# Kernel optimization log

Measured on AMD Instinct MI355X. Metric: run time of the kernel, lower is better.

## Reference

```python
import jax, jax.numpy as jnp
import numpy as np
from jax import lax

LEAK = 0.2  # LeakyReLU negative slope used both in flow_conv and as act_type


def conv2d(x, w, b):
    # x: (N,Cin,H,W), w: (Cout,Cin,kh,kw) -> 'SAME' padding, stride 1
    out = lax.conv_general_dilated(x, w, (1, 1), 'SAME',
                                   dimension_numbers=('NCHW', 'OIHW', 'NCHW'))
    return out + b[None, :, None, None]


def leaky(x):
    return jnp.where(x >= 0, x, LEAK * x)


def bilinear_sample(im, ix, iy):
    # im: (C,H,W); ix,iy: (H,W) absolute pixel coords; zero padding (grid_sample default)
    C, H, W = im.shape
    x0 = jnp.floor(ix)
    y0 = jnp.floor(iy)

    def gather(xi, yi):
        valid = (xi >= 0) & (xi <= W - 1) & (yi >= 0) & (yi <= H - 1)
        xc = jnp.clip(xi, 0, W - 1).astype(jnp.int32)
        yc = jnp.clip(yi, 0, H - 1).astype(jnp.int32)
        return im[:, yc, xc] * valid[None].astype(im.dtype)

    wx1 = ix - x0
    wy1 = iy - y0
    wx0 = 1.0 - wx1
    wy0 = 1.0 - wy1
    return (gather(x0, y0) * (wx0 * wy0)[None]
            + gather(x0 + 1, y0) * (wx1 * wy0)[None]
            + gather(x0, y0 + 1) * (wx0 * wy1)[None]
            + gather(x0 + 1, y0 + 1) * (wx1 * wy1)[None])


def warp_all(h, flows):
    # h: (B,Ch,H,W); flows: (B,L,2,H,W). Matches warp(prev_h, -flow) with
    # torch F.grid_sample (bilinear, zero padding, align_corners=False).
    B, Ch, H, W = h.shape
    dt = h.dtype
    xx = jnp.arange(W, dtype=dt)
    yy = jnp.arange(H, dtype=dt)
    vx = xx[None, None, None, :] - flows[:, :, 0]  # grid + (-flow), x coord
    vy = yy[None, None, :, None] - flows[:, :, 1]
    xn = 2.0 * vx / max(W - 1, 1) - 1.0  # normalize to [-1,1]
    yn = 2.0 * vy / max(H - 1, 1) - 1.0
    ix = ((xn + 1.0) * W - 1.0) * 0.5  # unnormalize, align_corners=False
    iy = ((yn + 1.0) * H - 1.0) * 0.5
    samp = jax.vmap(jax.vmap(bilinear_sample, in_axes=(None, 0, 0)),
                    in_axes=(0, 0, 0))
    out = samp(h, ix, iy)  # (B,L,Ch,H,W)
    return out.reshape(B, -1, H, W)  # (B, L*Ch, H, W), same order as torch.cat


def setup_inputs() -> dict:
    key = jax.random.key(0)
    ks = jax.random.split(key, 8)
    B, S, C, H, W = 4, 6, 8, 96, 96
    Ch, L = 64, 13
    sc = lambda fan_in: 1.0 / np.sqrt(fan_in)
    return {
        'inputs': jax.random.normal(ks[0], (B, S, C, H, W), jnp.float32),
        'states': jnp.zeros((B, Ch, H, W), jnp.float32),
        'fw1': jax.random.normal(ks[1], (32, C + Ch, 3, 3), jnp.float32) * sc((C + Ch) * 9),
        'fb1': jnp.zeros((32,), jnp.float32),
        'fw2': jax.random.normal(ks[2], (2 * L, 32, 3, 3), jnp.float32) * sc(32 * 9),
        'fb2': jnp.zeros((2 * L,), jnp.float32),
        'i2h_w': jax.random.normal(ks[3], (3 * Ch, C, 3, 3), jnp.float32) * sc(C * 9),
        'i2h_b': jnp.zeros((3 * Ch,), jnp.float32),
        'ret_w': jax.random.normal(ks[4], (3 * Ch, L * Ch, 1, 1), jnp.float32) * sc(L * Ch),
        'ret_b': jnp.zeros((3 * Ch,), jnp.float32),
        'seq_len': 6,
    }


def reference(inputs, states, fw1, fb1, fw2, fb2, i2h_w, i2h_b, ret_w, ret_b, seq_len):
    B, S, C, H, W = inputs.shape
    Ch = states.shape[1]
    # precompute i2h over all timesteps (as in the torch module)
    i2h = conv2d(inputs.reshape(B * S, C, H, W), i2h_w, i2h_b)
    i2h = i2h.reshape(B, S, 3 * Ch, H, W)

    def step(h, xs):
        x_t, i2h_t = xs  # (B,C,H,W), (B,3Ch,H,W)
        f = leaky(conv2d(jnp.concatenate([x_t, h], axis=1), fw1, fb1))
        flows = conv2d(f, fw2, fb2)  # (B, 2L, H, W)
        flows = flows.reshape(B, flows.shape[1] // 2, 2, H, W)
        warped = warp_all(h, flows)  # (B, L*Ch, H, W)
        h2h = conv2d(warped, ret_w, ret_b)  # (B, 3Ch, H, W)
        i1, i2, i3 = jnp.split(i2h_t, 3, axis=1)
        h1, h2, h3 = jnp.split(h2h, 3, axis=1)
        r = jax.nn.sigmoid(i1 + h1)
        u = jax.nn.sigmoid(i2 + h2)
        m = leaky(i3 + r * h3)
        nh = u * h + (1.0 - u) * m
        return nh, nh

    xs = (jnp.moveaxis(inputs, 0, 1), jnp.moveaxis(i2h, 0, 1))  # time-major
    last_h, outs = lax.scan(step, states, xs)
    return jnp.moveaxis(outs, 0, 1), last_h  # ((B,S,Ch,H,W), (B,Ch,H,W))
```

## Files before the change

kernel.cpp:

```cpp
#include <hip/hip_runtime.h>
#include <hip/hip_bf16.h>
#include <math.h>

#define Bn 4
#define Sn 6
#define Cin 8
#define Hh 96
#define Ww 96
#define HW (Hh*Ww)
#define Chn 64
#define Ln 13
#define LCh (Ln*Chn)
#define OC3 (3*Chn)
#define LEAK 0.2f

typedef __hip_bfloat16 bf16;
typedef __attribute__((ext_vector_type(8))) short short8v;
typedef __attribute__((ext_vector_type(4))) short short4v;
typedef __attribute__((ext_vector_type(4))) float f32x4;

__device__ __forceinline__ float b2f(bf16 v){ return __bfloat162float(v); }
__device__ __forceinline__ bf16  f2b(float v){ return __float2bfloat16(v); }
__device__ __forceinline__ unsigned short bbits(bf16 v){ union{bf16 b; unsigned short s;} u; u.b=v; return u.s; }
__device__ __forceinline__ float us2f(unsigned short u){
    union{unsigned int i; float f;} x; x.i = ((unsigned)u)<<16; return x.f;
}

__device__ __forceinline__ int4 mk_meta(float fx, float fy, int xc, int y){
    float ix = ((float)xc - fx) * (96.0f/95.0f) - 0.5f;
    float iy = ((float)y  - fy) * (96.0f/95.0f) - 0.5f;
    float x0f = floorf(ix), y0f = floorf(iy);
    float wx1 = ix - x0f,  wy1 = iy - y0f;
    float wx0 = 1.f - wx1, wy0 = 1.f - wy1;
    float vx0 = (x0f >=  0.f && x0f <= 95.f) ? 1.f : 0.f;
    float vx1 = (x0f >= -1.f && x0f <= 94.f) ? 1.f : 0.f;
    float vy0 = (y0f >=  0.f && y0f <= 95.f) ? 1.f : 0.f;
    float vy1 = (y0f >= -1.f && y0f <= 94.f) ? 1.f : 0.f;
    int xi0 = (int)fminf(fmaxf(x0f,      0.f), 95.f);
    int xi1 = (int)fminf(fmaxf(x0f+1.f,  0.f), 95.f);
    int yi0 = (int)fminf(fmaxf(y0f,      0.f), 95.f);
    int yi1 = (int)fminf(fmaxf(y0f+1.f,  0.f), 95.f);
    union { _Float16 h[2]; int i; } pz, pw;
    pz.h[0] = (_Float16)(wx0*wy0*vx0*vy0);
    pz.h[1] = (_Float16)(wx1*wy0*vx1*vy0);
    pw.h[0] = (_Float16)(wx0*wy1*vx0*vy1);
    pw.h[1] = (_Float16)(wx1*wy1*vx1*vy1);
    int4 m;
    m.x = (yi0*Ww+xi0) | ((yi0*Ww+xi1)<<16);
    m.y = (yi1*Ww+xi0) | ((yi1*Ww+xi1)<<16);
    m.z = pz.i; m.w = pw.i;
    return m;
}

__global__ void k_prep(const float* __restrict__ fw1, const float* __restrict__ fw2,
                       const float* __restrict__ wi,  const float* __restrict__ rw,
                       bf16* __restrict__ W1b, bf16* __restrict__ W2b,
                       bf16* __restrict__ Wi,  bf16* __restrict__ Wb)
{
    int i = blockIdx.x*256 + threadIdx.x;
    if (i < 21504){
        int oc = i/672, k = i%672; float v = 0.f;
        if (k < 648){ int tap = k/72, ic = k%72; v = fw1[(size_t)oc*648 + ic*9 + tap]; }
        W1b[i] = f2b(v);
    } else if (i < 30720){
        int j = i-21504; int oc = j/288, k = j%288; float v = 0.f;
        if (oc < 26){ int tap = k/32, ic = k%32; v = fw2[(size_t)oc*288 + ic*9 + tap]; }
        W2b[j] = f2b(v);
    } else if (i < 49152){
        int j = i-30720; int oc = j/96, k = j%96; float v = 0.f;
        if (k < 72){ int tap = k/8, ic = k%8; v = wi[(size_t)oc*72 + ic*9 + tap]; }
        Wi[j] = f2b(v);
    } else if (i < 208896){
        int j = i-49152; Wb[j] = f2b(rw[j]);
    }
}

__global__ void k_packx(const float* __restrict__ x, bf16* __restrict__ x_hwc)
{
    __shared__ unsigned short tx[8][68];
    int bs = blockIdx.y, pix0 = blockIdx.x*64, tid = threadIdx.x;
    #pragma unroll
    for (int it=0; it<2; ++it){
        int idx = it*256 + tid, ic = idx>>6, p = idx&63;
        tx[ic][p] = bbits(f2b(x[((size_t)bs*Cin + ic)*HW + pix0 + p]));
    }
    __syncthreads();
    unsigned short* dst = (unsigned short*)x_hwc;
    #pragma unroll
    for (int it=0; it<2; ++it){
        int j = it*256 + tid, p = j>>3, c = j&7;
        dst[((size_t)bs*HW + pix0 + p)*8 + c] = tx[c][p];
    }
}

__global__ void k_packh0(const float* __restrict__ s, bf16* __restrict__ hwc)
{
    __shared__ unsigned short t[64][65];
    int b = blockIdx.y, pix0 = blockIdx.x*64, tid = threadIdx.x;
    unsigned short* dst = (unsigned short*)hwc;
    #pragma unroll
    for (int it=0; it<16; ++it){
        int idx = it*256 + tid, c = idx>>6, p = idx&63;
        t[c][p] = bbits(f2b(s[((size_t)b*Chn + c)*HW + pix0 + p]));
    }
    __syncthreads();
    #pragma unroll
    for (int it=0; it<16; ++it){
        int idx = it*256 + tid, p = idx>>6, c = idx&63;
        dst[((size_t)b*HW + pix0 + p)*Chn + c] = t[c][p];
    }
}

__global__ __launch_bounds__(384) void k_front(const bf16* __restrict__ x_hwc,
        const bf16* __restrict__ h_hwc,
        const bf16* __restrict__ Wi,  const float* __restrict__ ib,
        const bf16* __restrict__ W1b, const float* __restrict__ fb1,
        bf16* __restrict__ i2h_hwc, bf16* __restrict__ f_hwc, int t)
{
    __shared__ bf16 tile[3*98*72];
    int y = blockIdx.x, b = blockIdx.y, tid = threadIdx.x;
    const bf16* xb = x_hwc + (size_t)(b*Sn + t)*HW*8;
    const bf16* hb = h_hwc + (size_t)b*HW*64;
    for (int s = tid; s < 294; s += 384){
        int r = s/98, px = s%98 - 1, yy = y + r - 1;
        float4* dst = (float4*)&tile[s*72];
        if (yy>=0 && yy<Hh && px>=0 && px<Ww){
            size_t gp = (size_t)yy*Ww + px;
            dst[0] = *(const float4*)(xb + gp*8);
            const float4* hsrc = (const float4*)(hb + gp*64);
            #pragma unroll
            for (int q=0;q<8;++q) dst[1+q] = hsrc[q];
        } else {
            float4 z{0,0,0,0};
            #pragma unroll
            for (int q=0;q<9;++q) dst[q] = z;
        }
    }
    __syncthreads();
    int wv = tid>>6, lane = tid&63, x0 = wv*16, n = lane&15, kg = lane>>4;
    int pix = y*Ww + x0 + n;

    {
        f32x4 acc[12];
        #pragma unroll
        for (int m=0;m<12;++m) acc[m] = f32x4{0,0,0,0};
        #pragma unroll
        for (int kk=0; kk<3; ++kk){
            int g = kk*4 + kg;
            int tap = (g > 8) ? 8 : g;
            int dy = tap/3, dx = tap%3;
            short8v bv = *(const short8v*)&tile[((dy*98) + (x0+n) + dx)*72];
            #pragma unroll
            for (int m=0;m<12;++m){
                short8v av = *(const short8v*)(Wi + (size_t)(m*16 + n)*96 + g*8);
                acc[m] = __builtin_amdgcn_mfma_f32_16x16x32_bf16(av, bv, acc[m], 0,0,0);
            }
        }
        size_t prow = ((size_t)b*HW + pix)*192;
        #pragma unroll
        for (int m=0;m<12;++m){
            short4v sv;
            #pragma unroll
            for (int r=0;r<4;++r){
                int oc = m*16 + kg*4 + r;
                sv[r] = (short)bbits(f2b(acc[m][r] + ib[oc]));
            }
            *(short4v*)&i2h_hwc[prow + m*16 + kg*4] = sv;
        }
    }

    {
        f32x4 acc0{0,0,0,0}, acc1{0,0,0,0};
        #pragma unroll
        for (int kk=0; kk<21; ++kk){
            int g = kk*4 + kg;
            int gc = (g > 80) ? 80 : g;
            int tap = gc/9, ch0 = (gc%9)*8;
            int dy = tap/3, dx = tap%3;
            short8v bv = *(const short8v*)&tile[(((dy*98) + (x0+n) + dx))*72 + ch0];
            short8v a0 = *(const short8v*)(W1b + (size_t)n*672 + g*8);
            short8v a1 = *(const short8v*)(W1b + (size_t)(16+n)*672 + g*8);
            acc0 = __builtin_amdgcn_mfma_f32_16x16x32_bf16(a0, bv, acc0, 0,0,0);
            acc1 = __builtin_amdgcn_mfma_f32_16x16x32_bf16(a1, bv, acc1, 0,0,0);
        }
        size_t prow = (size_t)b*HW + pix;
        #pragma unroll
        for (int mt=0; mt<2; ++mt){
            f32x4 a = mt ? acc1 : acc0;
            short4v sv;
            #pragma unroll
            for (int r=0;r<4;++r){
                int oc = mt*16 + kg*4 + r;
                float v = a[r] + fb1[oc];
                sv[r] = (short)bbits(f2b((v >= 0.f) ? v : LEAK*v));
            }
            *(short4v*)&f_hwc[prow*32 + mt*16 + kg*4] = sv;
        }
    }
}

__global__ __launch_bounds__(384) void k_conv2meta(const bf16* __restrict__ f_hwc,
        const bf16* __restrict__ W2b, const float* __restrict__ fb2,
        int4* __restrict__ meta)
{
    __shared__ bf16 tile[3*98*32];
    int y = blockIdx.x, b = blockIdx.y, tid = threadIdx.x;
    const bf16* fb = f_hwc + (size_t)b*HW*32;
    for (int s = tid; s < 294; s += 384){
        int r = s/98, px = s%98 - 1, yy = y + r - 1;
        float4* dst = (float4*)&tile[s*32];
        if (yy>=0 && yy<Hh && px>=0 && px<Ww){
            const float4* src = (const float4*)(fb + ((size_t)yy*Ww + px)*32);
            #pragma unroll
            for (int q=0;q<4;++q) dst[q] = src[q];
        } else {
            float4 z{0,0,0,0};
            #pragma unroll
            for (int q=0;q<4;++q) dst[q] = z;
        }
    }
    __syncthreads();
    int wv = tid>>6, lane = tid&63, x0 = wv*16, n = lane&15, kg = lane>>4;
    f32x4 acc0{0,0,0,0}, acc1{0,0,0,0};
    #pragma unroll
    for (int kk=0; kk<9; ++kk){
        int g = kk*4 + kg;
        int tap = g>>2, ch0 = (g&3)*8;
        int dy = tap/3, dx = tap%3;
        short8v bv = *(const short8v*)&tile[(((dy*98) + (x0+n) + dx))*32 + ch0];
        short8v a0 = *(const short8v*)(W2b + (size_t)n*288 + g*8);
        short8v a1 = *(const short8v*)(W2b + (size_t)(16+n)*288 + g*8);
        acc0 = __builtin_amdgcn_mfma_f32_16x16x32_bf16(a0, bv, acc0, 0,0,0);
        acc1 = __builtin_amdgcn_mfma_f32_16x16x32_bf16(a1, bv, acc1, 0,0,0);
    }
    int xc = x0 + n, pix = y*Ww + xc;
    int4* mb = meta + (size_t)b*Ln*HW + pix;
    {
        float v0 = acc0[0] + fb2[kg*4+0], v1 = acc0[1] + fb2[kg*4+1];
        float v2 = acc0[2] + fb2[kg*4+2], v3 = acc0[3] + fb2[kg*4+3];
        mb[(size_t)(2*kg  )*HW] = mk_meta(v0, v1, xc, y);
        mb[(size_t)(2*kg+1)*HW] = mk_meta(v2, v3, xc, y);
    }
    if (kg < 3){
        float v0 = acc1[0] + fb2[16+kg*4+0], v1 = acc1[1] + fb2[16+kg*4+1];
        mb[(size_t)(8+2*kg)*HW] = mk_meta(v0, v1, xc, y);
        if (kg < 2){
            float v2 = acc1[2] + fb2[16+kg*4+2], v3 = acc1[3] + fb2[16+kg*4+3];
            mb[(size_t)(9+2*kg)*HW] = mk_meta(v2, v3, xc, y);
        }
    }
}

__global__ __launch_bounds__(256) void k_fused(const int4* __restrict__ meta,
        const bf16* __restrict__ h_cur, const bf16* __restrict__ Wb,
        const float* __restrict__ rb, const bf16* __restrict__ i2h_hwc,
        bf16* __restrict__ h_nxt, float* __restrict__ out, int t)
{
    __shared__ bf16 wlds[32*LCh];
    char* ldsb = (char*)wlds;
    int tid = threadIdx.x, wv = tid>>6, lane = tid&63;
    int b = blockIdx.y, pix0 = blockIdx.x*32;
    const bf16* hb = h_cur + (size_t)b*HW*64;
    const unsigned short* hsu = (const unsigned short*)hb;
    const int4* mb = meta + (size_t)b*Ln*HW + pix0;
    int c = lane;

    for (int l=0; l<13; ++l){
        int4 mm[8];
        #pragma unroll
        for (int j=0;j<8;++j) mm[j] = mb[(size_t)l*HW + wv + 4*j];
        unsigned short g0[8], g1[8], g2[8], g3[8];
        #pragma unroll
        for (int j=0;j<8;++j){
            int o00 = mm[j].x & 0xFFFF, o10 = ((unsigned)mm[j].x) >> 16;
            int o01 = mm[j].y & 0xFFFF, o11 = ((unsigned)mm[j].y) >> 16;
            g0[j] = hsu[(size_t)o00*64 + c];
            g1[j] = hsu[(size_t)o10*64 + c];
            g2[j] = hsu[(size_t)o01*64 + c];
            g3[j] = hsu[(size_t)o11*64 + c];
        }
        #pragma unroll
        for (int j=0;j<8;++j){
            union { int i; _Float16 h[2]; } uz, uw;
            uz.i = mm[j].z; uw.i = mm[j].w;
            float v = us2f(g0[j])*(float)uz.h[0] + us2f(g1[j])*(float)uz.h[1]
                    + us2f(g2[j])*(float)uw.h[0] + us2f(g3[j])*(float)uw.h[1];
            int px = wv + 4*j;
            int off = px*1664 + (((l*64 + c)*2) ^ ((px&7)<<4));
            *(bf16*)(ldsb + off) = f2b(v);
        }
    }

    int col = lane & 15, kg = lane >> 4;
    int pxa = pix0 + col, pxb = pxa + 16;
    short4v hva = *(const short4v*)&hb[(size_t)pxa*64 + wv*16 + kg*4];
    short4v hvb = *(const short4v*)&hb[(size_t)pxb*64 + wv*16 + kg*4];
    const bf16* ia = i2h_hwc + ((size_t)b*HW + pxa)*192 + wv*16 + kg*4;
    const bf16* ibp= i2h_hwc + ((size_t)b*HW + pxb)*192 + wv*16 + kg*4;
    short4v i1a = *(const short4v*)(ia);
    short4v i2a = *(const short4v*)(ia + 64);
    short4v i3a = *(const short4v*)(ia + 128);
    short4v i1b = *(const short4v*)(ibp);
    short4v i2b = *(const short4v*)(ibp + 64);
    short4v i3b = *(const short4v*)(ibp + 128);
    __syncthreads();

    const short8v* a0 = (const short8v*)(Wb + (size_t)((wv+0)*16+col)*LCh + kg*8);
    const short8v* a1 = (const short8v*)(Wb + (size_t)((wv+4)*16+col)*LCh + kg*8);
    const short8v* a2 = (const short8v*)(Wb + (size_t)((wv+8)*16+col)*LCh + kg*8);
    f32x4 c0a{0,0,0,0}, c1a{0,0,0,0}, c2a{0,0,0,0};
    f32x4 c0b{0,0,0,0}, c1b{0,0,0,0}, c2b{0,0,0,0};
    int swz = (col&7)<<4;
    #pragma unroll 2
    for (int kk=0; kk<26; ++kk){
        short8v av0 = a0[kk*4], av1 = a1[kk*4], av2 = a2[kk*4];
        int offa = col*1664 + ((kk*64 + kg*16) ^ swz);
        int offb = (col+16)*1664 + ((kk*64 + kg*16) ^ swz);
        short8v bva = *(const short8v*)(ldsb + offa);
        short8v bvb = *(const short8v*)(ldsb + offb);
        c0a = __builtin_amdgcn_mfma_f32_16x16x32_bf16(av0, bva, c0a, 0,0,0);
        c0b = __builtin_amdgcn_mfma_f32_16x16x32_bf16(av0, bvb, c0b, 0,0,0);
        c1a = __builtin_amdgcn_mfma_f32_16x16x32_bf16(av1, bva, c1a, 0,0,0);
        c1b = __builtin_amdgcn_mfma_f32_16x16x32_bf16(av1, bvb, c1b, 0,0,0);
        c2a = __builtin_amdgcn_mfma_f32_16x16x32_bf16(av2, bva, c2a, 0,0,0);
        c2b = __builtin_amdgcn_mfma_f32_16x16x32_bf16(av2, bvb, c2b, 0,0,0);
    }

    float nha[4], nhb[4];
    #pragma unroll
    for (int r=0; r<4; ++r){
        int cc = wv*16 + kg*4 + r;
        float h1 = c0a[r] + rb[cc];
        float h2 = c1a[r] + rb[cc+64];
        float h3 = c2a[r] + rb[cc+128];
        float rg = 1.f/(1.f + expf(-(us2f((unsigned short)i1a[r]) + h1)));
        float u  = 1.f/(1.f + expf(-(us2f((unsigned short)i2a[r]) + h2)));
        float mp = us2f((unsigned short)i3a[r]) + rg*h3;
        float m  = (mp >= 0.f) ? mp : LEAK*mp;
        float nh = u*us2f((unsigned short)hva[r]) + (1.f - u)*m;
        nha[r] = nh;
        out[(((size_t)(b*Sn+t))*Chn + cc)*HW + pxa] = nh;
        if (t == Sn-1)
            out[(size_t)Bn*Sn*Chn*HW + ((size_t)b*Chn + cc)*HW + pxa] = nh;
    }
    #pragma unroll
    for (int r=0; r<4; ++r){
        int cc = wv*16 + kg*4 + r;
        float h1 = c0b[r] + rb[cc];
        float h2 = c1b[r] + rb[cc+64];
        float h3 = c2b[r] + rb[cc+128];
        float rg = 1.f/(1.f + expf(-(us2f((unsigned short)i1b[r]) + h1)));
        float u  = 1.f/(1.f + expf(-(us2f((unsigned short)i2b[r]) + h2)));
        float mp = us2f((unsigned short)i3b[r]) + rg*h3;
        float m  = (mp >= 0.f) ? mp : LEAK*mp;
        float nh = u*us2f((unsigned short)hvb[r]) + (1.f - u)*m;
        nhb[r] = nh;
        out[(((size_t)(b*Sn+t))*Chn + cc)*HW + pxb] = nh;
        if (t == Sn-1)
            out[(size_t)Bn*Sn*Chn*HW + ((size_t)b*Chn + cc)*HW + pxb] = nh;
    }

    __syncthreads();
    bf16* htr = wlds;
    #pragma unroll
    for (int r=0; r<4; ++r){
        htr[col*72      + wv*16 + kg*4 + r] = f2b(nha[r]);
        htr[(col+16)*72 + wv*16 + kg*4 + r] = f2b(nhb[r]);
    }
    __syncthreads();
    int px2 = tid >> 3, cg = tid & 7;
    short8v ho8 = *(short8v*)&htr[px2*72 + cg*8];
    *(short8v*)&h_nxt[((size_t)b*HW + pix0 + px2)*64 + cg*8] = ho8;
}

extern "C" void kernel_launch(void* const* d_in, const int* in_sizes, int n_in,
                              void* d_out, int out_size, void* d_ws, size_t ws_size,
                              hipStream_t stream) {
    const float* inputs = (const float*)d_in[0];
    const float* states = (const float*)d_in[1];
    const float* fw1    = (const float*)d_in[2];
    const float* fb1    = (const float*)d_in[3];
    const float* fw2    = (const float*)d_in[4];
    const float* fb2    = (const float*)d_in[5];
    const float* i2h_w  = (const float*)d_in[6];
    const float* i2h_b  = (const float*)d_in[7];
    const float* ret_w  = (const float*)d_in[8];
    const float* ret_b  = (const float*)d_in[9];
    float* out = (float*)d_out;

    char* ws = (char*)d_ws;
    bf16* h_hwcA  = (bf16*)(ws);
    bf16* h_hwcB  = (bf16*)(ws +  4718592);
    bf16* x_hwc   = (bf16*)(ws +  9437184);
    bf16* i2h_hwc = (bf16*)(ws + 12976128);
    bf16* f_hwc   = (bf16*)(ws + 27131904);
    int4* meta    = (int4*)(ws + 29491200);
    bf16* W1b     = (bf16*)(ws + 37158912);
    bf16* W2b     = (bf16*)(ws + 37201920);
    bf16* Wi      = (bf16*)(ws + 37220352);
    bf16* Wb      = (bf16*)(ws + 37257216);

    k_prep  <<<dim3(816),        256, 0, stream>>>(fw1, fw2, i2h_w, ret_w,
                                                   W1b, W2b, Wi, Wb);
    k_packx <<<dim3(144, Bn*Sn), 256, 0, stream>>>(inputs, x_hwc);
    k_packh0<<<dim3(144, Bn),    256, 0, stream>>>(states, h_hwcA);

    bf16* h_cur = h_hwcA;
    bf16* h_nxt = h_hwcB;
    for (int t = 0; t < Sn; ++t) {
        k_front    <<<dim3(96, Bn),  384, 0, stream>>>(x_hwc, h_cur, Wi, i2h_b,
                                                       W1b, fb1, i2h_hwc, f_hwc, t);
        k_conv2meta<<<dim3(96, Bn),  384, 0, stream>>>(f_hwc, W2b, fb2, meta);
        k_fused    <<<dim3(288, Bn), 256, 0, stream>>>(meta, h_cur, Wb, ret_b,
                                                       i2h_hwc, h_nxt, out, t);
        bf16* tmp = h_cur; h_cur = h_nxt; h_nxt = tmp;
    }
}
```

Before: 709.8 us.

## Double-buffer warped tiles per flow and interleave gather with MFMA accumulation

The fused warp+h2h kernel no longer stages all 13 warped feature slices into one large LDS array before the GEMM. It now keeps two small per-flow LDS tiles. Each iteration issues the global gathers for the next flow while running the MFMAs on the current tile, and one barrier separates the two buffers. This cuts LDS per block from roughly 53KB to 8KB, which should raise occupancy, and it overlaps gather latency with matrix work. The cost is one barrier per flow step, and each pixel-wave now handles a contiguous run of 8 pixels instead of strided ones.

```diff
diff --git a/kernel.cpp b/kernel.cpp
--- a/kernel.cpp
+++ b/kernel.cpp
@@ -256,19 +256,27 @@
         const float* __restrict__ rb, const bf16* __restrict__ i2h_hwc,
         bf16* __restrict__ h_nxt, float* __restrict__ out, int t)
 {
-    __shared__ bf16 wlds[32*LCh];
-    char* ldsb = (char*)wlds;
+    __shared__ bf16 buf[2][32*64];
     int tid = threadIdx.x, wv = tid>>6, lane = tid&63;
     int b = blockIdx.y, pix0 = blockIdx.x*32;
     const bf16* hb = h_cur + (size_t)b*HW*64;
     const unsigned short* hsu = (const unsigned short*)hb;
     const int4* mb = meta + (size_t)b*Ln*HW + pix0;
     int c = lane;
-
-    for (int l=0; l<13; ++l){
+    int col = lane & 15, kg = lane >> 4;
+    int swz = (col&7)<<4;
+
+    const bf16* arow0 = Wb + (size_t)((wv+0)*16+col)*LCh + kg*8;
+    const bf16* arow1 = Wb + (size_t)((wv+4)*16+col)*LCh + kg*8;
+    const bf16* arow2 = Wb + (size_t)((wv+8)*16+col)*LCh + kg*8;
+
+    f32x4 c0a{0,0,0,0}, c1a{0,0,0,0}, c2a{0,0,0,0};
+    f32x4 c0b{0,0,0,0}, c1b{0,0,0,0}, c2b{0,0,0,0};
+
+    {
         int4 mm[8];
         #pragma unroll
-        for (int j=0;j<8;++j) mm[j] = mb[(size_t)l*HW + wv + 4*j];
+        for (int j=0;j<8;++j) mm[j] = mb[wv*8 + j];
         unsigned short g0[8], g1[8], g2[8], g3[8];
         #pragma unroll
         for (int j=0;j<8;++j){
@@ -279,19 +287,81 @@
             g2[j] = hsu[(size_t)o01*64 + c];
             g3[j] = hsu[(size_t)o11*64 + c];
         }
+        char* dst = (char*)buf[0];
         #pragma unroll
         for (int j=0;j<8;++j){
             union { int i; _Float16 h[2]; } uz, uw;
             uz.i = mm[j].z; uw.i = mm[j].w;
             float v = us2f(g0[j])*(float)uz.h[0] + us2f(g1[j])*(float)uz.h[1]
                     + us2f(g2[j])*(float)uw.h[0] + us2f(g3[j])*(float)uw.h[1];
-            int px = wv + 4*j;
-            int off = px*1664 + (((l*64 + c)*2) ^ ((px&7)<<4));
-            *(bf16*)(ldsb + off) = f2b(v);
-        }
-    }
-
-    int col = lane & 15, kg = lane >> 4;
+            int px = wv*8 + j;
+            *(bf16*)(dst + px*128 + ((c*2) ^ ((px&7)<<4))) = f2b(v);
+        }
+    }
+
+    for (int l=0; l<13; ++l){
+        const bf16* a0p = arow0 + l*64;
+        const bf16* a1p = arow1 + l*64;
+        const bf16* a2p = arow2 + l*64;
+        short8v av00 = *(const short8v*)(a0p);
+        short8v av01 = *(const short8v*)(a0p + 32);
+        short8v av10 = *(const short8v*)(a1p);
+        short8v av11 = *(const short8v*)(a1p + 32);
+        short8v av20 = *(const short8v*)(a2p);
+        short8v av21 = *(const short8v*)(a2p + 32);
+
+        int4 mm[8];
+        unsigned short g0[8], g1[8], g2[8], g3[8];
+        if (l < 12){
+            #pragma unroll
+            for (int j=0;j<8;++j) mm[j] = mb[(size_t)(l+1)*HW + wv*8 + j];
+            #pragma unroll
+            for (int j=0;j<8;++j){
+                int o00 = mm[j].x & 0xFFFF, o10 = ((unsigned)mm[j].x) >> 16;
+                int o01 = mm[j].y & 0xFFFF, o11 = ((unsigned)mm[j].y) >> 16;
+                g0[j] = hsu[(size_t)o00*64 + c];
+                g1[j] = hsu[(size_t)o10*64 + c];
+                g2[j] = hsu[(size_t)o01*64 + c];
+                g3[j] = hsu[(size_t)o11*64 + c];
+            }
+        }
+
+        __syncthreads();
+
+        {
+            char* cur = (char*)buf[l&1];
+            short8v bva0 = *(const short8v*)(cur + col*128      + ((kg*16)      ^ swz));
+            short8v bvb0 = *(const short8v*)(cur + (col+16)*128 + ((kg*16)      ^ swz));
+            short8v bva1 = *(const short8v*)(cur + col*128      + ((64 + kg*16) ^ swz));
+            short8v bvb1 = *(const short8v*)(cur + (col+16)*128 + ((64 + kg*16) ^ swz));
+            c0a = __builtin_amdgcn_mfma_f32_16x16x32_bf16(av00, bva0, c0a, 0,0,0);
+            c0b = __builtin_amdgcn_mfma_f32_16x16x32_bf16(av00, bvb0, c0b, 0,0,0);
+            c1a = __builtin_amdgcn_mfma_f32_16x16x32_bf16(av10, bva0, c1a, 0,0,0);
+            c1b = __builtin_amdgcn_mfma_f32_16x16x32_bf16(av10, bvb0, c1b, 0,0,0);
+            c2a = __builtin_amdgcn_mfma_f32_16x16x32_bf16(av20, bva0, c2a, 0,0,0);
+            c2b = __builtin_amdgcn_mfma_f32_16x16x32_bf16(av20, bvb0, c2b, 0,0,0);
+            c0a = __builtin_amdgcn_mfma_f32_16x16x32_bf16(av01, bva1, c0a, 0,0,0);
+            c0b = __builtin_amdgcn_mfma_f32_16x16x32_bf16(av01, bvb1, c0b, 0,0,0);
+            c1a = __builtin_amdgcn_mfma_f32_16x16x32_bf16(av11, bva1, c1a, 0,0,0);
+            c1b = __builtin_amdgcn_mfma_f32_16x16x32_bf16(av11, bvb1, c1b, 0,0,0);
+            c2a = __builtin_amdgcn_mfma_f32_16x16x32_bf16(av21, bva1, c2a, 0,0,0);
+            c2b = __builtin_amdgcn_mfma_f32_16x16x32_bf16(av21, bvb1, c2b, 0,0,0);
+        }
+
+        if (l < 12){
+            char* dst = (char*)buf[(l+1)&1];
+            #pragma unroll
+            for (int j=0;j<8;++j){
+                union { int i; _Float16 h[2]; } uz, uw;
+                uz.i = mm[j].z; uw.i = mm[j].w;
+                float v = us2f(g0[j])*(float)uz.h[0] + us2f(g1[j])*(float)uz.h[1]
+                        + us2f(g2[j])*(float)uw.h[0] + us2f(g3[j])*(float)uw.h[1];
+                int px = wv*8 + j;
+                *(bf16*)(dst + px*128 + ((c*2) ^ ((px&7)<<4))) = f2b(v);
+            }
+        }
+    }
+
     int pxa = pix0 + col, pxb = pxa + 16;
     short4v hva = *(const short4v*)&hb[(size_t)pxa*64 + wv*16 + kg*4];
     short4v hvb = *(const short4v*)&hb[(size_t)pxb*64 + wv*16 + kg*4];
@@ -303,28 +373,6 @@
     short4v i1b = *(const short4v*)(ibp);
     short4v i2b = *(const short4v*)(ibp + 64);
     short4v i3b = *(const short4v*)(ibp + 128);
-    __syncthreads();
-
-    const short8v* a0 = (const short8v*)(Wb + (size_t)((wv+0)*16+col)*LCh + kg*8);
-    const short8v* a1 = (const short8v*)(Wb + (size_t)((wv+4)*16+col)*LCh + kg*8);
-    const short8v* a2 = (const short8v*)(Wb + (size_t)((wv+8)*16+col)*LCh + kg*8);
-    f32x4 c0a{0,0,0,0}, c1a{0,0,0,0}, c2a{0,0,0,0};
-    f32x4 c0b{0,0,0,0}, c1b{0,0,0,0}, c2b{0,0,0,0};
-    int swz = (col&7)<<4;
-    #pragma unroll 2
-    for (int kk=0; kk<26; ++kk){
-        short8v av0 = a0[kk*4], av1 = a1[kk*4], av2 = a2[kk*4];
-        int offa = col*1664 + ((kk*64 + kg*16) ^ swz);
-        int offb = (col+16)*1664 + ((kk*64 + kg*16) ^ swz);
-        short8v bva = *(const short8v*)(ldsb + offa);
-        short8v bvb = *(const short8v*)(ldsb + offb);
-        c0a = __builtin_amdgcn_mfma_f32_16x16x32_bf16(av0, bva, c0a, 0,0,0);
-        c0b = __builtin_amdgcn_mfma_f32_16x16x32_bf16(av0, bvb, c0b, 0,0,0);
-        c1a = __builtin_amdgcn_mfma_f32_16x16x32_bf16(av1, bva, c1a, 0,0,0);
-        c1b = __builtin_amdgcn_mfma_f32_16x16x32_bf16(av1, bvb, c1b, 0,0,0);
-        c2a = __builtin_amdgcn_mfma_f32_16x16x32_bf16(av2, bva, c2a, 0,0,0);
-        c2b = __builtin_amdgcn_mfma_f32_16x16x32_bf16(av2, bvb, c2b, 0,0,0);
-    }
 
     float nha[4], nhb[4];
     #pragma unroll
@@ -361,15 +409,16 @@
     }
 
     __syncthreads();
-    bf16* htr = wlds;
+    char* htr = (char*)buf[0];
     #pragma unroll
     for (int r=0; r<4; ++r){
-        htr[col*72      + wv*16 + kg*4 + r] = f2b(nha[r]);
-        htr[(col+16)*72 + wv*16 + kg*4 + r] = f2b(nhb[r]);
+        int cc = wv*16 + kg*4 + r;
+        *(bf16*)(htr + col*128      + ((cc*2) ^ ((col&7)<<4)))      = f2b(nha[r]);
+        *(bf16*)(htr + (col+16)*128 + ((cc*2) ^ ((col&7)<<4)))      = f2b(nhb[r]);
     }
     __syncthreads();
     int px2 = tid >> 3, cg = tid & 7;
-    short8v ho8 = *(short8v*)&htr[px2*72 + cg*8];
+    short8v ho8 = *(const short8v*)(htr + px2*128 + ((cg*16) ^ ((px2&7)<<4)));
     *(short8v*)&h_nxt[((size_t)b*HW + pix0 + px2)*64 + cg*8] = ho8;
 }
 
```

New measurement: 725.8 us. +2.3%, slower.

## Split fused warp+h2h kernel into separate warp and GEMM kernels per batch

Applied to the files above, without the earlier changes.

Replaces the single fused kernel, which built the warped tensor in shared memory and ran the MFMA GEMM on it, with two kernels per batch item. The first gathers bilinear samples into a global warped buffer using scalar (readfirstlane) metadata. The second runs the h2h GEMM with B operands read directly from global memory and applies the GRU update. The goal is more parallelism and less LDS pressure per block, at the cost of a global round trip for the warped tensor (about 15 MB per batch) and many more kernel launches.

```diff
diff --git a/kernel.cpp b/kernel.cpp
--- a/kernel.cpp
+++ b/kernel.cpp
@@ -24,6 +24,12 @@
 __device__ __forceinline__ unsigned short bbits(bf16 v){ union{bf16 b; unsigned short s;} u; u.b=v; return u.s; }
 __device__ __forceinline__ float us2f(unsigned short u){
     union{unsigned int i; float f;} x; x.i = ((unsigned)u)<<16; return x.f;
+}
+__device__ __forceinline__ const int4* rfl_ptr(const int4* p){
+    uintptr_t v = (uintptr_t)p;
+    int lo = __builtin_amdgcn_readfirstlane((int)(v & 0xFFFFFFFFu));
+    int hi = __builtin_amdgcn_readfirstlane((int)(v >> 32));
+    return (const int4*)(((uintptr_t)(unsigned)hi << 32) | (unsigned)lo);
 }
 
 __device__ __forceinline__ int4 mk_meta(float fx, float fy, int xc, int y){
@@ -251,82 +257,70 @@
     }
 }
 
-__global__ __launch_bounds__(256) void k_fused(const int4* __restrict__ meta,
-        const bf16* __restrict__ h_cur, const bf16* __restrict__ Wb,
-        const float* __restrict__ rb, const bf16* __restrict__ i2h_hwc,
-        bf16* __restrict__ h_nxt, float* __restrict__ out, int t)
-{
-    __shared__ bf16 wlds[32*LCh];
-    char* ldsb = (char*)wlds;
+__global__ __launch_bounds__(256) void k_warp(const int4* __restrict__ meta,
+        const bf16* __restrict__ h_cur, bf16* __restrict__ warped, int b)
+{
+    int tid = threadIdx.x, wv = tid>>6, c = tid&63;
+    int l = blockIdx.y;
+    int pix0 = blockIdx.x*32 + wv*8;
+    const unsigned short* hsu = (const unsigned short*)(h_cur + (size_t)b*HW*64);
+    const int4* mwp = rfl_ptr(meta + (size_t)b*Ln*HW + (size_t)l*HW + pix0);
+
+    int mz[8], mw[8];
+    unsigned short g0[8], g1[8], g2[8], g3[8];
+    #pragma unroll
+    for (int j=0;j<8;++j){
+        int4 m = mwp[j];
+        int sx = __builtin_amdgcn_readfirstlane(m.x);
+        int sy = __builtin_amdgcn_readfirstlane(m.y);
+        mz[j] = __builtin_amdgcn_readfirstlane(m.z);
+        mw[j] = __builtin_amdgcn_readfirstlane(m.w);
+        g0[j] = hsu[(size_t)(sx & 0xFFFF)*64 + c];
+        g1[j] = hsu[(size_t)((unsigned)sx >> 16)*64 + c];
+        g2[j] = hsu[(size_t)(sy & 0xFFFF)*64 + c];
+        g3[j] = hsu[(size_t)((unsigned)sy >> 16)*64 + c];
+    }
+    #pragma unroll
+    for (int j=0;j<8;++j){
+        union { int i; _Float16 h[2]; } uz, uw;
+        uz.i = mz[j]; uw.i = mw[j];
+        float v = us2f(g0[j])*(float)uz.h[0] + us2f(g1[j])*(float)uz.h[1]
+                + us2f(g2[j])*(float)uw.h[0] + us2f(g3[j])*(float)uw.h[1];
+        warped[(size_t)(pix0+j)*LCh + l*64 + c] = f2b(v);
+    }
+}
+
+__global__ __launch_bounds__(256) void k_h2h(const bf16* __restrict__ warped,
+        const bf16* __restrict__ Wb, const float* __restrict__ rb,
+        const bf16* __restrict__ i2h_hwc, const bf16* __restrict__ h_cur,
+        bf16* __restrict__ h_nxt, float* __restrict__ out, int b, int t)
+{
     int tid = threadIdx.x, wv = tid>>6, lane = tid&63;
-    int b = blockIdx.y, pix0 = blockIdx.x*32;
+    int col = lane & 15, kg = lane >> 4;
+    int pix0 = blockIdx.x*16;
+    int pxa = pix0 + col;
     const bf16* hb = h_cur + (size_t)b*HW*64;
-    const unsigned short* hsu = (const unsigned short*)hb;
-    const int4* mb = meta + (size_t)b*Ln*HW + pix0;
-    int c = lane;
-
-    for (int l=0; l<13; ++l){
-        int4 mm[8];
-        #pragma unroll
-        for (int j=0;j<8;++j) mm[j] = mb[(size_t)l*HW + wv + 4*j];
-        unsigned short g0[8], g1[8], g2[8], g3[8];
-        #pragma unroll
-        for (int j=0;j<8;++j){
-            int o00 = mm[j].x & 0xFFFF, o10 = ((unsigned)mm[j].x) >> 16;
-            int o01 = mm[j].y & 0xFFFF, o11 = ((unsigned)mm[j].y) >> 16;
-            g0[j] = hsu[(size_t)o00*64 + c];
-            g1[j] = hsu[(size_t)o10*64 + c];
-            g2[j] = hsu[(size_t)o01*64 + c];
-            g3[j] = hsu[(size_t)o11*64 + c];
-        }
-        #pragma unroll
-        for (int j=0;j<8;++j){
-            union { int i; _Float16 h[2]; } uz, uw;
-            uz.i = mm[j].z; uw.i = mm[j].w;
-            float v = us2f(g0[j])*(float)uz.h[0] + us2f(g1[j])*(float)uz.h[1]
-                    + us2f(g2[j])*(float)uw.h[0] + us2f(g3[j])*(float)uw.h[1];
-            int px = wv + 4*j;
-            int off = px*1664 + (((l*64 + c)*2) ^ ((px&7)<<4));
-            *(bf16*)(ldsb + off) = f2b(v);
-        }
-    }
-
-    int col = lane & 15, kg = lane >> 4;
-    int pxa = pix0 + col, pxb = pxa + 16;
+
     short4v hva = *(const short4v*)&hb[(size_t)pxa*64 + wv*16 + kg*4];
-    short4v hvb = *(const short4v*)&hb[(size_t)pxb*64 + wv*16 + kg*4];
     const bf16* ia = i2h_hwc + ((size_t)b*HW + pxa)*192 + wv*16 + kg*4;
-    const bf16* ibp= i2h_hwc + ((size_t)b*HW + pxb)*192 + wv*16 + kg*4;
     short4v i1a = *(const short4v*)(ia);
     short4v i2a = *(const short4v*)(ia + 64);
     short4v i3a = *(const short4v*)(ia + 128);
-    short4v i1b = *(const short4v*)(ibp);
-    short4v i2b = *(const short4v*)(ibp + 64);
-    short4v i3b = *(const short4v*)(ibp + 128);
-    __syncthreads();
-
+
+    const short8v* bp = (const short8v*)(warped + (size_t)pxa*LCh + kg*8);
     const short8v* a0 = (const short8v*)(Wb + (size_t)((wv+0)*16+col)*LCh + kg*8);
     const short8v* a1 = (const short8v*)(Wb + (size_t)((wv+4)*16+col)*LCh + kg*8);
     const short8v* a2 = (const short8v*)(Wb + (size_t)((wv+8)*16+col)*LCh + kg*8);
     f32x4 c0a{0,0,0,0}, c1a{0,0,0,0}, c2a{0,0,0,0};
-    f32x4 c0b{0,0,0,0}, c1b{0,0,0,0}, c2b{0,0,0,0};
-    int swz = (col&7)<<4;
     #pragma unroll 2
     for (int kk=0; kk<26; ++kk){
-        short8v av0 = a0[kk*4], av1 = a1[kk*4], av2 = a2[kk*4];
-        int offa = col*1664 + ((kk*64 + kg*16) ^ swz);
-        int offb = (col+16)*1664 + ((kk*64 + kg*16) ^ swz);
-        short8v bva = *(const short8v*)(ldsb + offa);
-        short8v bvb = *(const short8v*)(ldsb + offb);
-        c0a = __builtin_amdgcn_mfma_f32_16x16x32_bf16(av0, bva, c0a, 0,0,0);
-        c0b = __builtin_amdgcn_mfma_f32_16x16x32_bf16(av0, bvb, c0b, 0,0,0);
-        c1a = __builtin_amdgcn_mfma_f32_16x16x32_bf16(av1, bva, c1a, 0,0,0);
-        c1b = __builtin_amdgcn_mfma_f32_16x16x32_bf16(av1, bvb, c1b, 0,0,0);
-        c2a = __builtin_amdgcn_mfma_f32_16x16x32_bf16(av2, bva, c2a, 0,0,0);
-        c2b = __builtin_amdgcn_mfma_f32_16x16x32_bf16(av2, bvb, c2b, 0,0,0);
-    }
-
-    float nha[4], nhb[4];
+        short8v bv = bp[kk*4];
+        c0a = __builtin_amdgcn_mfma_f32_16x16x32_bf16(a0[kk*4], bv, c0a, 0,0,0);
+        c1a = __builtin_amdgcn_mfma_f32_16x16x32_bf16(a1[kk*4], bv, c1a, 0,0,0);
+        c2a = __builtin_amdgcn_mfma_f32_16x16x32_bf16(a2[kk*4], bv, c2a, 0,0,0);
+    }
+
+    float nha[4];
     #pragma unroll
     for (int r=0; r<4; ++r){
         int cc = wv*16 + kg*4 + r;
@@ -343,34 +337,10 @@
         if (t == Sn-1)
             out[(size_t)Bn*Sn*Chn*HW + ((size_t)b*Chn + cc)*HW + pxa] = nh;
     }
-    #pragma unroll
-    for (int r=0; r<4; ++r){
-        int cc = wv*16 + kg*4 + r;
-        float h1 = c0b[r] + rb[cc];
-        float h2 = c1b[r] + rb[cc+64];
-        float h3 = c2b[r] + rb[cc+128];
-        float rg = 1.f/(1.f + expf(-(us2f((unsigned short)i1b[r]) + h1)));
-        float u  = 1.f/(1.f + expf(-(us2f((unsigned short)i2b[r]) + h2)));
-        float mp = us2f((unsigned short)i3b[r]) + rg*h3;
-        float m  = (mp >= 0.f) ? mp : LEAK*mp;
-        float nh = u*us2f((unsigned short)hvb[r]) + (1.f - u)*m;
-        nhb[r] = nh;
-        out[(((size_t)(b*Sn+t))*Chn + cc)*HW + pxb] = nh;
-        if (t == Sn-1)
-            out[(size_t)Bn*Sn*Chn*HW + ((size_t)b*Chn + cc)*HW + pxb] = nh;
-    }
-
-    __syncthreads();
-    bf16* htr = wlds;
-    #pragma unroll
-    for (int r=0; r<4; ++r){
-        htr[col*72      + wv*16 + kg*4 + r] = f2b(nha[r]);
-        htr[(col+16)*72 + wv*16 + kg*4 + r] = f2b(nhb[r]);
-    }
-    __syncthreads();
-    int px2 = tid >> 3, cg = tid & 7;
-    short8v ho8 = *(short8v*)&htr[px2*72 + cg*8];
-    *(short8v*)&h_nxt[((size_t)b*HW + pix0 + px2)*64 + cg*8] = ho8;
+    short4v sva;
+    #pragma unroll
+    for (int r=0; r<4; ++r) sva[r] = (short)bbits(f2b(nha[r]));
+    *(short4v*)&h_nxt[((size_t)b*HW + pxa)*64 + wv*16 + kg*4] = sva;
 }
 
 extern "C" void kernel_launch(void* const* d_in, const int* in_sizes, int n_in,
@@ -399,6 +369,7 @@
     bf16* W2b     = (bf16*)(ws + 37201920);
     bf16* Wi      = (bf16*)(ws + 37220352);
     bf16* Wb      = (bf16*)(ws + 37257216);
+    bf16* warped  = (bf16*)(ws + 37576704);
 
     k_prep  <<<dim3(816),        256, 0, stream>>>(fw1, fw2, i2h_w, ret_w,
                                                    W1b, W2b, Wi, Wb);
@@ -411,8 +382,11 @@
         k_front    <<<dim3(96, Bn),  384, 0, stream>>>(x_hwc, h_cur, Wi, i2h_b,
                                                        W1b, fb1, i2h_hwc, f_hwc, t);
         k_conv2meta<<<dim3(96, Bn),  384, 0, stream>>>(f_hwc, W2b, fb2, meta);
-        k_fused    <<<dim3(288, Bn), 256, 0, stream>>>(meta, h_cur, Wb, ret_b,
-                                                       i2h_hwc, h_nxt, out, t);
+        for (int b = 0; b < Bn; ++b) {
+            k_warp<<<dim3(288, Ln), 256, 0, stream>>>(meta, h_cur, warped, b);
+            k_h2h <<<dim3(576),     256, 0, stream>>>(warped, Wb, ret_b, i2h_hwc,
+                                                      h_cur, h_nxt, out, b, t);
+        }
         bf16* tmp = h_cur; h_cur = h_nxt; h_nxt = tmp;
     }
 }
```

New measurement: 1.453 ms. 2.05x slower.

## Vectorize warp gather with 16-byte channel loads and write h_nxt directly

Applied to the files above, without the earlier changes.

The bilinear warp gather is remapped so each thread handles one pixel and loads 8 contiguous bf16 channels per corner as a 16-byte vector, in place of one 2-byte scalar per lane. Each wave now covers a subset of the 13 flow levels, and results are written to LDS as 16-byte swizzled stores. The epilogue drops the LDS transpose and its two barriers, storing 4-channel bf16 vectors straight to h_nxt. The aim is fewer, wider global and LDS transactions. The cost is uneven level work across waves (13 levels over 4 waves) and narrower 8-byte stores for h_nxt.

```diff
diff --git a/kernel.cpp b/kernel.cpp
--- a/kernel.cpp
+++ b/kernel.cpp
@@ -263,31 +263,39 @@
     const bf16* hb = h_cur + (size_t)b*HW*64;
     const unsigned short* hsu = (const unsigned short*)hb;
     const int4* mb = meta + (size_t)b*Ln*HW + pix0;
-    int c = lane;
-
-    for (int l=0; l<13; ++l){
-        int4 mm[8];
-        #pragma unroll
-        for (int j=0;j<8;++j) mm[j] = mb[(size_t)l*HW + wv + 4*j];
-        unsigned short g0[8], g1[8], g2[8], g3[8];
-        #pragma unroll
-        for (int j=0;j<8;++j){
-            int o00 = mm[j].x & 0xFFFF, o10 = ((unsigned)mm[j].x) >> 16;
-            int o01 = mm[j].y & 0xFFFF, o11 = ((unsigned)mm[j].y) >> 16;
-            g0[j] = hsu[(size_t)o00*64 + c];
-            g1[j] = hsu[(size_t)o10*64 + c];
-            g2[j] = hsu[(size_t)o01*64 + c];
-            g3[j] = hsu[(size_t)o11*64 + c];
-        }
-        #pragma unroll
-        for (int j=0;j<8;++j){
-            union { int i; _Float16 h[2]; } uz, uw;
-            uz.i = mm[j].z; uw.i = mm[j].w;
-            float v = us2f(g0[j])*(float)uz.h[0] + us2f(g1[j])*(float)uz.h[1]
-                    + us2f(g2[j])*(float)uw.h[0] + us2f(g3[j])*(float)uw.h[1];
-            int px = wv + 4*j;
-            int off = px*1664 + (((l*64 + c)*2) ^ ((px&7)<<4));
-            *(bf16*)(ldsb + off) = f2b(v);
+
+    int px = lane & 31;
+    int oh = lane >> 5;
+    int pswz = (px&7)<<4;
+    for (int l = wv; l < Ln; l += 4){
+        int4 m = mb[(size_t)l*HW + px];
+        int o00 = m.x & 0xFFFF, o10 = ((unsigned)m.x) >> 16;
+        int o01 = m.y & 0xFFFF, o11 = ((unsigned)m.y) >> 16;
+        union { int i; _Float16 h[2]; } uz, uw;
+        uz.i = m.z; uw.i = m.w;
+        float w00 = (float)uz.h[0], w10 = (float)uz.h[1];
+        float w01 = (float)uw.h[0], w11 = (float)uw.h[1];
+        #pragma unroll
+        for (int o2 = 0; o2 < 4; ++o2){
+            int oct = o2*2 + oh;
+            const unsigned short* s00 = hsu + (size_t)o00*64 + oct*8;
+            const unsigned short* s10 = hsu + (size_t)o10*64 + oct*8;
+            const unsigned short* s01 = hsu + (size_t)o01*64 + oct*8;
+            const unsigned short* s11 = hsu + (size_t)o11*64 + oct*8;
+            short8v v00 = *(const short8v*)s00;
+            short8v v10 = *(const short8v*)s10;
+            short8v v01 = *(const short8v*)s01;
+            short8v v11 = *(const short8v*)s11;
+            short8v r8;
+            #pragma unroll
+            for (int k=0;k<8;++k){
+                float v = us2f((unsigned short)v00[k])*w00
+                        + us2f((unsigned short)v10[k])*w10
+                        + us2f((unsigned short)v01[k])*w01
+                        + us2f((unsigned short)v11[k])*w11;
+                r8[k] = (short)bbits(f2b(v));
+            }
+            *(short8v*)(ldsb + px*1664 + ((l*128 + oct*16) ^ pswz)) = r8;
         }
     }
 
@@ -315,7 +323,7 @@
     for (int kk=0; kk<26; ++kk){
         short8v av0 = a0[kk*4], av1 = a1[kk*4], av2 = a2[kk*4];
         int offa = col*1664 + ((kk*64 + kg*16) ^ swz);
-        int offb = (col+16)*1664 + ((kk*64 + kg*16) ^ swz);
+        int offb = (col+16)*1664 + ((kk*64 + kg*16) ^ ((col&7)<<4));
         short8v bva = *(const short8v*)(ldsb + offa);
         short8v bvb = *(const short8v*)(ldsb + offb);
         c0a = __builtin_amdgcn_mfma_f32_16x16x32_bf16(av0, bva, c0a, 0,0,0);
@@ -359,18 +367,14 @@
         if (t == Sn-1)
             out[(size_t)Bn*Sn*Chn*HW + ((size_t)b*Chn + cc)*HW + pxb] = nh;
     }
-
-    __syncthreads();
-    bf16* htr = wlds;
+    short4v sva, svb;
     #pragma unroll
     for (int r=0; r<4; ++r){
-        htr[col*72      + wv*16 + kg*4 + r] = f2b(nha[r]);
-        htr[(col+16)*72 + wv*16 + kg*4 + r] = f2b(nhb[r]);
-    }
-    __syncthreads();
-    int px2 = tid >> 3, cg = tid & 7;
-    short8v ho8 = *(short8v*)&htr[px2*72 + cg*8];
-    *(short8v*)&h_nxt[((size_t)b*HW + pix0 + px2)*64 + cg*8] = ho8;
+        sva[r] = (short)bbits(f2b(nha[r]));
+        svb[r] = (short)bbits(f2b(nhb[r]));
+    }
+    *(short4v*)&h_nxt[((size_t)b*HW + pxa)*64 + wv*16 + kg*4] = sva;
+    *(short4v*)&h_nxt[((size_t)b*HW + pxb)*64 + wv*16 + kg*4] = svb;
 }
 
 extern "C" void kernel_launch(void* const* d_in, const int* in_sizes, int n_in,
```

After: 722.3 us. Within noise of the previous version (+1.8%).
